# Optimization experiments

Measured on AMD Instinct MI355X. Metric: run time of the kernel, lower is better.

## Reference

```python
import jax, jax.numpy as jnp
import numpy as np

B = 1024
E = 512
NUM_HEADS = 8
EPS = 1e-5  # torch LayerNorm default


def _mha(x, w_qkv, b_qkv, w_o, b_o):
    """torch nn.MultiheadAttention (batch_first, self-attn, no dropout).
    x: [N, S, E]; w_qkv: [3E, E]; w_o: [E, E]."""
    N, S, Ex = x.shape
    H = NUM_HEADS
    D = Ex // H
    qkv = x @ w_qkv.T + b_qkv                      # [N, S, 3E]
    q, k, v = jnp.split(qkv, 3, axis=-1)
    q = q.reshape(N, S, H, D).transpose(0, 2, 1, 3)  # [N, H, S, D]
    k = k.reshape(N, S, H, D).transpose(0, 2, 1, 3)
    v = v.reshape(N, S, H, D).transpose(0, 2, 1, 3)
    scores = jnp.einsum('nhqd,nhkd->nhqk', q, k) * (D ** -0.5)
    attn = jax.nn.softmax(scores, axis=-1)
    out = jnp.einsum('nhqk,nhkd->nhqd', attn, v)
    out = out.transpose(0, 2, 1, 3).reshape(N, S, Ex)
    return out @ w_o.T + b_o


def _box_perm(g):
    """Permute 9x9 grid so each 3x3 box becomes a contiguous row of 9.
    This permutation is its own inverse. g: [B, 9, 9, E]."""
    Bx = g.shape[0]
    return (g.reshape(Bx, 3, 3, 3, 3, E)
             .transpose(0, 1, 3, 2, 4, 5)
             .reshape(Bx, 9, 9, E))


def setup_inputs() -> dict:
    key = jax.random.key(0)
    ks = jax.random.split(key, 16)
    s = 0.02
    inp = {'x': jax.random.normal(ks[0], (B, 81, E), jnp.float32)}
    for i, p in enumerate(['row', 'col', 'box']):
        inp[p + '_wqkv'] = jax.random.normal(ks[1 + 2 * i], (3 * E, E), jnp.float32) * s
        inp[p + '_bqkv'] = jnp.zeros((3 * E,), jnp.float32)
        inp[p + '_wo'] = jax.random.normal(ks[2 + 2 * i], (E, E), jnp.float32) * s
        inp[p + '_bo'] = jnp.zeros((E,), jnp.float32)
    inp['w1'] = jax.random.normal(ks[7], (2 * E, 3 * E), jnp.float32) * s
    inp['b1'] = jnp.zeros((2 * E,), jnp.float32)
    inp['w2'] = jax.random.normal(ks[8], (E, 2 * E), jnp.float32) * s
    inp['b2'] = jnp.zeros((E,), jnp.float32)
    inp['gamma'] = jnp.ones((E,), jnp.float32)
    inp['beta'] = jnp.zeros((E,), jnp.float32)
    return inp


def reference(x, row_wqkv, row_bqkv, row_wo, row_bo,
              col_wqkv, col_bqkv, col_wo, col_bo,
              box_wqkv, box_bqkv, box_wo, box_bo,
              w1, b1, w2, b2, gamma, beta):
    Bx = x.shape[0]
    # Row attention: rows are already contiguous groups of 9.
    row_out = _mha(x.reshape(Bx * 9, 9, E), row_wqkv, row_bqkv, row_wo, row_bo)
    row_out = row_out.reshape(Bx, 81, E)
    # Column attention: transpose grid so columns are contiguous.
    col_x = x.reshape(Bx, 9, 9, E).transpose(0, 2, 1, 3).reshape(Bx * 9, 9, E)
    col_out = _mha(col_x, col_wqkv, col_bqkv, col_wo, col_bo)
    col_out = col_out.reshape(Bx, 9, 9, E).transpose(0, 2, 1, 3).reshape(Bx, 81, E)
    # Box attention: permute grid so each 3x3 box is contiguous.
    box_x = _box_perm(x.reshape(Bx, 9, 9, E)).reshape(Bx * 9, 9, E)
    box_out = _mha(box_x, box_wqkv, box_bqkv, box_wo, box_bo)
    box_out = _box_perm(box_out.reshape(Bx, 9, 9, E)).reshape(Bx, 81, E)
    # Constraint mixer MLP.
    combined = jnp.concatenate([row_out, col_out, box_out], axis=-1)  # [B,81,3E]
    h = jax.nn.gelu(combined @ w1.T + b1, approximate=False)
    mixed = h @ w2.T + b2
    # Residual + LayerNorm.
    y = x + mixed
    mu = jnp.mean(y, axis=-1, keepdims=True)
    var = jnp.var(y, axis=-1, keepdims=True)
    return (y - mu) * jax.lax.rsqrt(var + EPS) * gamma + beta
```

## Files before the change

### kernel.cpp

```cpp
#include <hip/hip_runtime.h>
#include <hip/hip_bf16.h>
#include <math.h>

typedef __hip_bfloat16 bf16;
typedef __attribute__((ext_vector_type(8))) short s8v;
typedef __attribute__((ext_vector_type(4))) short s4v;
typedef __attribute__((ext_vector_type(4))) float f4v;

static __device__ __forceinline__ float bfs2f(short s) {
    return __uint_as_float(((unsigned)(unsigned short)s) << 16);
}
static __device__ __forceinline__ short f2bfs(float f) {
    __hip_bfloat16 h = __float2bfloat16(f);
    return *reinterpret_cast<short*>(&h);
}

__global__ __launch_bounds__(256)
void cvt_f32_bf16(const float* __restrict__ in, bf16* __restrict__ out, long n4)
{
    const long i = (long)blockIdx.x * 256 + threadIdx.x;
    if (i >= n4) return;
    const float4 v = reinterpret_cast<const float4*>(in)[i];
    s4v o;
    o[0] = f2bfs(v.x); o[1] = f2bfs(v.y); o[2] = f2bfs(v.z); o[3] = f2bfs(v.w);
    reinterpret_cast<s4v*>(out)[i] = o;
}

__global__ __launch_bounds__(256)
void cvt_t_f32_bf16(const float* __restrict__ in, bf16* __restrict__ out,
                    int R, int C)
{
    __shared__ float t[32][33];
    const int bx = blockIdx.x * 32;
    const int by = blockIdx.y * 32;
    const int tx = threadIdx.x & 31;
    const int ty = threadIdx.x >> 5;
#pragma unroll
    for (int r = ty; r < 32; r += 8)
        t[r][tx] = in[(long)(by + r) * C + bx + tx];
    __syncthreads();
#pragma unroll
    for (int r = ty; r < 32; r += 8)
        out[(long)(bx + r) * R + by + tx] = __float2bfloat16(t[tx][r]);
}

__global__ __launch_bounds__(256)
void fold_b1(const float* __restrict__ w1, const float* __restrict__ bo0,
             const float* __restrict__ bo1, const float* __restrict__ bo2,
             const float* __restrict__ b1, float* __restrict__ b1p)
{
    const int m = blockIdx.x * 256 + threadIdx.x;
    float s = b1[m];
    const float* w = w1 + (long)m * 1536;
    for (int k = 0; k < 512; ++k) s += w[k]        * bo0[k];
    for (int k = 0; k < 512; ++k) s += w[512 + k]  * bo1[k];
    for (int k = 0; k < 512; ++k) s += w[1024 + k] * bo2[k];
    b1p[m] = s;
}

template<int ACT>
__global__ __launch_bounds__(512, 2)
void gemm256(const bf16* __restrict__ A, const bf16* __restrict__ B,
             const float* __restrict__ bias, bf16* __restrict__ C,
             int K, int lda, int ldc, int coff)
{
    __shared__ __align__(16) bf16 sA[2][256 * 64];
    __shared__ __align__(16) bf16 sB[2][256 * 64];
    const int tid  = threadIdx.x;
    const int lane = tid & 63;
    const int wid  = tid >> 6;
    const int nwg  = gridDim.x * gridDim.y;
    const int orig = blockIdx.x + gridDim.x * blockIdx.y;
    const int q = nwg >> 3, r = nwg & 7, xcd = orig & 7;
    const int sb = (xcd < r ? xcd * (q + 1) : r * (q + 1) + (xcd - r) * q) + (orig >> 3);
    const int bCol = sb % gridDim.x;
    const int bRow = sb / gridDim.x;

    const int wr  = (wid >> 2) * 128;
    const int wc  = (wid & 3) * 64;
    const int fr  = lane & 15;
    const int hi4 = lane >> 4;
    const int rx  = fr & 7;

    f4v acc[8][4];
#pragma unroll
    for (int i = 0; i < 8; ++i)
#pragma unroll
        for (int j = 0; j < 4; ++j) acc[i][j] = (f4v)(0.0f);

    const int srow = tid >> 3;
    const int scol = ((tid & 7) ^ (srow & 7)) * 8;
    const bf16* Abase = A + (long)(bRow * 256 + srow) * lda + scol;
    const bf16* Bbase = B + (long)(bCol * 256 + srow) * K + scol;

#define GL16(src, dst)                                                          \
    __builtin_amdgcn_global_load_lds(                                           \
        (const __attribute__((address_space(1))) unsigned int*)(src),           \
        (__attribute__((address_space(3))) unsigned int*)(dst), 16, 0, 0)

#define STAGE_A(h, tt, bc) do {                                                 \
    const bf16* g_ = Abase + (long)(h) * 128 * lda + (long)(tt) * 64;           \
    char* d_ = (char*)sA[bc] + (h) * 16384 + tid * 16;                          \
    GL16(g_, d_); GL16(g_ + 64 * (long)lda, d_ + 8192); } while (0)

#define STAGE_B(h, tt, bc) do {                                                 \
    const bf16* g_ = Bbase + (long)(h) * 128 * K + (long)(tt) * 64;             \
    char* d_ = (char*)sB[bc] + (h) * 16384 + tid * 16;                          \
    GL16(g_, d_); GL16(g_ + 64 * (long)K, d_ + 8192); } while (0)

#define LDSW(base, row, kk)                                                     \
    (*(const s8v*)((base) + (row) * 128 + ((((kk) * 4 + hi4) ^ rx) << 4)))

    const int nk = K >> 6;

    STAGE_A(0, 0, 0); STAGE_A(1, 0, 0);
    STAGE_B(0, 0, 0); STAGE_B(1, 0, 0);
    STAGE_B(0, 1, 1); STAGE_B(1, 1, 1);
    asm volatile("s_waitcnt vmcnt(4)" ::: "memory");
    __builtin_amdgcn_s_barrier();
    __builtin_amdgcn_sched_barrier(0);

    for (int t = 0; t < nk; ++t) {
        const int c = t & 1;
        const char* sAc = (const char*)sA[c];
        const char* sBc = (const char*)sB[c];
        s8v bfr[4][2];

        {
            s8v af0[2][2], af1[2][2];
#pragma unroll
            for (int m2 = 0; m2 < 2; ++m2)
#pragma unroll
                for (int kk = 0; kk < 2; ++kk) {
                    af0[m2][kk] = LDSW(sAc, wr + m2 * 16 + fr, kk);
                    af1[m2][kk] = LDSW(sAc, wr + (2 + m2) * 16 + fr, kk);
                }
#pragma unroll
            for (int ni = 0; ni < 4; ++ni)
#pragma unroll
                for (int kk = 0; kk < 2; ++kk)
                    bfr[ni][kk] = LDSW(sBc, wc + ni * 16 + fr, kk);
            if (t + 1 < nk) { STAGE_A(0, t + 1, c ^ 1); STAGE_A(1, t + 1, c ^ 1); }
            __builtin_amdgcn_s_setprio(1);
#pragma unroll
            for (int kk = 0; kk < 2; ++kk)
#pragma unroll
                for (int m2 = 0; m2 < 2; ++m2)
#pragma unroll
                    for (int ni = 0; ni < 4; ++ni) {
                        acc[m2][ni] = __builtin_amdgcn_mfma_f32_16x16x32_bf16(
                            af0[m2][kk], bfr[ni][kk], acc[m2][ni], 0, 0, 0);
                        acc[2 + m2][ni] = __builtin_amdgcn_mfma_f32_16x16x32_bf16(
                            af1[m2][kk], bfr[ni][kk], acc[2 + m2][ni], 0, 0, 0);
                    }
            __builtin_amdgcn_s_setprio(0);
        }
        __builtin_amdgcn_s_barrier();

        {
            s8v af0[2][2], af1[2][2];
#pragma unroll
            for (int m2 = 0; m2 < 2; ++m2)
#pragma unroll
                for (int kk = 0; kk < 2; ++kk) {
                    af0[m2][kk] = LDSW(sAc, wr + (4 + m2) * 16 + fr, kk);
                    af1[m2][kk] = LDSW(sAc, wr + (6 + m2) * 16 + fr, kk);
                }
            if (t + 2 < nk) { STAGE_B(0, t + 2, c); STAGE_B(1, t + 2, c); }
            __builtin_amdgcn_s_setprio(1);
#pragma unroll
            for (int kk = 0; kk < 2; ++kk)
#pragma unroll
                for (int m2 = 0; m2 < 2; ++m2)
#pragma unroll
                    for (int ni = 0; ni < 4; ++ni) {
                        acc[4 + m2][ni] = __builtin_amdgcn_mfma_f32_16x16x32_bf16(
                            af0[m2][kk], bfr[ni][kk], acc[4 + m2][ni], 0, 0, 0);
                        acc[6 + m2][ni] = __builtin_amdgcn_mfma_f32_16x16x32_bf16(
                            af1[m2][kk], bfr[ni][kk], acc[6 + m2][ni], 0, 0, 0);
                    }
            __builtin_amdgcn_s_setprio(0);
        }
        if (t + 2 < nk) {
            asm volatile("s_waitcnt vmcnt(4)" ::: "memory");
        } else if (t + 1 < nk) {
            asm volatile("s_waitcnt vmcnt(0)" ::: "memory");
        }
        __builtin_amdgcn_s_barrier();
        __builtin_amdgcn_sched_barrier(0);
    }
#undef STAGE_A
#undef STAGE_B
#undef GL16
#undef LDSW

    const int frow = hi4 * 4;
    const long rowBase = (long)bRow * 256 + wr;
    const int  colBase = bCol * 256 + wc;
#pragma unroll
    for (int ni = 0; ni < 4; ++ni) {
        const int col = colBase + ni * 16 + fr;
        const float bi = bias ? bias[coff + col] : 0.0f;
#pragma unroll
        for (int mi = 0; mi < 8; ++mi) {
#pragma unroll
            for (int j = 0; j < 4; ++j) {
                float v = acc[mi][ni][j] + bi;
                if (ACT == 1) {
                    const float u = v * (0.7978845608f + 0.0356774081f * v * v);
                    const float tnh = 1.0f - 2.0f / (__expf(2.0f * u) + 1.0f);
                    v = 0.5f * v * (1.0f + tnh);
                }
                const long rr = rowBase + mi * 16 + frow + j;
                C[rr * (long)ldc + coff + col] = __float2bfloat16(v);
            }
        }
    }
}

__global__ __launch_bounds__(256)
void attn9(const bf16* __restrict__ qkv, bf16* __restrict__ outg,
           long chunk_base)
{
    __shared__ __align__(16) bf16 sQKV[9 * 1536];
    __shared__ float sP[8 * 81];
    __shared__ int sTok[9];
    const int tid = threadIdx.x;
    const int branch = blockIdx.y;
    const int bx = blockIdx.x;
    const int s = (bx & 7) * (2304 >> 3) + (bx >> 3);
    const int b = s / 9, g = s % 9;

    if (tid < 9) {
        const int p = tid;
        int cell;
        if (branch == 0)      cell = g * 9 + p;
        else if (branch == 1) cell = p * 9 + g;
        else                  cell = ((g / 3) * 3 + p / 3) * 9 + (g % 3) * 3 + (p % 3);
        sTok[p] = b * 81 + cell;
    }
    __syncthreads();

    const long brOff = (long)branch * 1536;
    for (int c = tid; c < 1728; c += 256) {
        const int p = c / 192;
        const int off = (c - p * 192) * 8;
        *(s8v*)(&sQKV[p * 1536 + off]) =
            *(const s8v*)(&qkv[(long)sTok[p] * 4608 + brOff + off]);
    }
    __syncthreads();

    for (int t = tid; t < 648; t += 256) {
        const int h = t / 81;
        const int r = t - h * 81;
        const int i = r / 9, j = r - (r / 9) * 9;
        const bf16* qp = &sQKV[i * 1536 + h * 64];
        const bf16* kp = &sQKV[j * 1536 + 512 + h * 64];
        float accd = 0.0f;
#pragma unroll
        for (int dc = 0; dc < 8; ++dc) {
            s8v qv = *(const s8v*)(qp + dc * 8);
            s8v kv = *(const s8v*)(kp + dc * 8);
#pragma unroll
            for (int e2 = 0; e2 < 8; ++e2)
                accd += bfs2f(qv[e2]) * bfs2f(kv[e2]);
        }
        sP[t] = accd * 0.125f;
    }
    __syncthreads();

    if (tid < 72) {
        float* row = &sP[tid * 9];
        float m = row[0];
#pragma unroll
        for (int j = 1; j < 9; ++j) m = fmaxf(m, row[j]);
        float sum = 0.f, e[9];
#pragma unroll
        for (int j = 0; j < 9; ++j) { e[j] = expf(row[j] - m); sum += e[j]; }
        const float inv = 1.0f / sum;
#pragma unroll
        for (int j = 0; j < 9; ++j) row[j] = e[j] * inv;
    }
    __syncthreads();

    for (int t = tid; t < 576; t += 256) {
        const int i = t >> 6;
        const int c8 = (t & 63) * 8;
        const int h = (t & 63) >> 3;
        const float* prow = &sP[h * 81 + i * 9];
        float accv[8];
#pragma unroll
        for (int q2 = 0; q2 < 8; ++q2) accv[q2] = 0.f;
#pragma unroll
        for (int j = 0; j < 9; ++j) {
            const float p = prow[j];
            s8v vv = *(const s8v*)(&sQKV[j * 1536 + 1024 + c8]);
#pragma unroll
            for (int q2 = 0; q2 < 8; ++q2)
                accv[q2] += p * bfs2f(vv[q2]);
        }
        s8v ov;
#pragma unroll
        for (int q2 = 0; q2 < 8; ++q2) ov[q2] = f2bfs(accv[q2]);
        *(s8v*)(&outg[(chunk_base + sTok[i]) * 1536 + branch * 512 + c8]) = ov;
    }
}

__global__ __launch_bounds__(256)
void ln_res(const float* __restrict__ x, const bf16* __restrict__ mixed,
            const float* __restrict__ gamma, const float* __restrict__ beta,
            float* __restrict__ out)
{
    const int tid = threadIdx.x;
    const int lane = tid & 63;
    const long row = (long)blockIdx.x * 4 + (tid >> 6);
    const long base = row * 512 + lane * 8;
    const float4 x0 = *(const float4*)(&x[base]);
    const float4 x1 = *(const float4*)(&x[base + 4]);
    const s8v mv = *(const s8v*)(&mixed[base]);
    float y[8];
    y[0] = x0.x + bfs2f(mv[0]); y[1] = x0.y + bfs2f(mv[1]);
    y[2] = x0.z + bfs2f(mv[2]); y[3] = x0.w + bfs2f(mv[3]);
    y[4] = x1.x + bfs2f(mv[4]); y[5] = x1.y + bfs2f(mv[5]);
    y[6] = x1.z + bfs2f(mv[6]); y[7] = x1.w + bfs2f(mv[7]);
    float sum = 0.f, sq = 0.f;
#pragma unroll
    for (int j = 0; j < 8; ++j) { sum += y[j]; sq += y[j] * y[j]; }
#pragma unroll
    for (int o = 32; o > 0; o >>= 1) {
        sum += __shfl_xor(sum, o, 64);
        sq  += __shfl_xor(sq, o, 64);
    }
    const float mean = sum * (1.f / 512.f);
    const float inv = rsqrtf(sq * (1.f / 512.f) - mean * mean + 1e-5f);
    const float4 g0 = *(const float4*)(&gamma[lane * 8]);
    const float4 g1 = *(const float4*)(&gamma[lane * 8 + 4]);
    const float4 b0 = *(const float4*)(&beta[lane * 8]);
    const float4 b1 = *(const float4*)(&beta[lane * 8 + 4]);
    float4 o0, o1;
    o0.x = (y[0] - mean) * inv * g0.x + b0.x;
    o0.y = (y[1] - mean) * inv * g0.y + b0.y;
    o0.z = (y[2] - mean) * inv * g0.z + b0.z;
    o0.w = (y[3] - mean) * inv * g0.w + b0.w;
    o1.x = (y[4] - mean) * inv * g1.x + b1.x;
    o1.y = (y[5] - mean) * inv * g1.y + b1.y;
    o1.z = (y[6] - mean) * inv * g1.z + b1.z;
    o1.w = (y[7] - mean) * inv * g1.w + b1.w;
    *(float4*)(&out[base]) = o0;
    *(float4*)(&out[base + 4]) = o1;
}

extern "C" void kernel_launch(void* const* d_in, const int* in_sizes, int n_in,
                              void* d_out, int out_size, void* d_ws, size_t ws_size,
                              hipStream_t stream)
{
    (void)in_sizes; (void)n_in; (void)out_size; (void)ws_size;
    const float* x     = (const float*)d_in[0];
    const float* w1f   = (const float*)d_in[13];
    const float* b1f   = (const float*)d_in[14];
    const float* b2f   = (const float*)d_in[16];
    const float* gamma = (const float*)d_in[17];
    const float* beta  = (const float*)d_in[18];

    char* ws = (char*)d_ws;
    bf16* attnall   = (bf16*)(ws);
    bf16* mixed     = (bf16*)(ws);
    char* R         = ws + 254803968LL;
    bf16* qkv3chunk = (bf16*)(R);
    bf16* xb        = (bf16*)(R + 191102976LL);
    bf16* h         = (bf16*)(R);
    char* wb        = ws + 530841600LL;
    long off = 0;
    bf16* wqkv3_b = (bf16*)(wb + off); off += 4718592;
    bf16* woT_b[3];
    for (int i = 0; i < 3; ++i) { woT_b[i] = (bf16*)(wb + off); off += 524288; }
    bf16* w1_b  = (bf16*)(wb + off); off += 3145728;
    bf16* w2_b  = (bf16*)(wb + off); off += 1048576;
    bf16* Wp    = (bf16*)(wb + off); off += 3145728;
    float* b1p  = (float*)(wb + off); off += 4096;
    float* bqkv3 = (float*)(wb + off); off += 18432;

    const dim3 blk(256, 1, 1);
    const dim3 blk512(512, 1, 1);

    cvt_f32_bf16<<<dim3(41472), blk, 0, stream>>>(x, xb, 10616832L);
    for (int i = 0; i < 3; ++i) {
        cvt_f32_bf16<<<dim3(768), blk, 0, stream>>>(
            (const float*)d_in[1 + i * 4], wqkv3_b + (long)i * 786432, 196608L);
        cvt_t_f32_bf16<<<dim3(16, 16), blk, 0, stream>>>(
            (const float*)d_in[3 + i * 4], woT_b[i], 512, 512);
        hipMemcpyAsync(bqkv3 + i * 1536, d_in[2 + i * 4], 1536 * sizeof(float),
                       hipMemcpyDeviceToDevice, stream);
    }
    cvt_f32_bf16<<<dim3(1536), blk, 0, stream>>>(w1f, w1_b, 393216L);
    cvt_f32_bf16<<<dim3(512), blk, 0, stream>>>((const float*)d_in[15], w2_b, 131072L);

    fold_b1<<<dim3(4), blk, 0, stream>>>(w1f, (const float*)d_in[4],
                                         (const float*)d_in[8], (const float*)d_in[12],
                                         b1f, b1p);

    for (int br = 0; br < 3; ++br)
        gemm256<0><<<dim3(2, 4), blk512, 0, stream>>>(
            w1_b + br * 512, woT_b[br], nullptr, Wp, 512, 1536, 1536, br * 512);

    const long ROWS_C = 20736;
    for (int c = 0; c < 4; ++c) {
        const bf16* xA = xb + c * ROWS_C * 512;
        gemm256<0><<<dim3(18, 81), blk512, 0, stream>>>(
            xA, wqkv3_b, bqkv3, qkv3chunk, 512, 512, 4608, 0);
        attn9<<<dim3(2304, 3), blk, 0, stream>>>(qkv3chunk, attnall, c * ROWS_C);
    }
    gemm256<1><<<dim3(4, 324), blk512, 0, stream>>>(attnall, Wp, b1p, h, 1536, 1536, 1024, 0);
    gemm256<0><<<dim3(2, 324), blk512, 0, stream>>>(h, w2_b, b2f, mixed, 1024, 1024, 512, 0);
    ln_res<<<dim3(20736), blk, 0, stream>>>(x, mixed, gamma, beta, (float*)d_out);
}
```

Measured before the change: 1.564 ms.

## Stage GEMM epilogue through LDS and split attn9 work per wave

```diff
diff --git a/kernel.cpp b/kernel.cpp
--- a/kernel.cpp
+++ b/kernel.cpp
@@ -194,6 +194,9 @@
 #undef GL16
 #undef LDSW
 
+    __syncthreads();
+    bf16* ep = (wid < 4) ? ((bf16*)sA + wid * 8192)
+                         : ((bf16*)sB + (wid - 4) * 8192);
     const int frow = hi4 * 4;
     const long rowBase = (long)bRow * 256 + wr;
     const int  colBase = bCol * 256 + wc;
@@ -211,66 +214,89 @@
                     const float tnh = 1.0f - 2.0f / (__expf(2.0f * u) + 1.0f);
                     v = 0.5f * v * (1.0f + tnh);
                 }
-                const long rr = rowBase + mi * 16 + frow + j;
-                C[rr * (long)ldc + coff + col] = __float2bfloat16(v);
+                ep[(mi * 16 + frow + j) * 64 + ni * 16 + fr] = __float2bfloat16(v);
             }
         }
     }
+    asm volatile("s_waitcnt lgkmcnt(0)" ::: "memory");
+    __builtin_amdgcn_sched_barrier(0);
+    const int lr8 = lane >> 3;
+    const int lc  = (lane & 7) * 8;
+#pragma unroll
+    for (int q2 = 0; q2 < 16; ++q2) {
+        const int lrow = q2 * 8 + lr8;
+        const s8v vv = *(const s8v*)(&ep[lrow * 64 + lc]);
+        *(s8v*)(&C[(rowBase + lrow) * (long)ldc + coff + colBase + lc]) = vv;
+    }
+}
+
+__device__ __forceinline__ int cell9(int branch, int g, int p)
+{
+    if (branch == 0) return g * 9 + p;
+    if (branch == 1) return p * 9 + g;
+    return ((g / 3) * 3 + p / 3) * 9 + (g % 3) * 3 + (p % 3);
 }
 
 __global__ __launch_bounds__(256)
 void attn9(const bf16* __restrict__ qkv, bf16* __restrict__ outg,
            long chunk_base)
 {
-    __shared__ __align__(16) bf16 sQKV[9 * 1536];
-    __shared__ float sP[8 * 81];
-    __shared__ int sTok[9];
-    const int tid = threadIdx.x;
+    __shared__ __align__(16) bf16 sW[4 * 9 * 392];
+    __shared__ float sP[4][2][84];
+    const int tid  = threadIdx.x;
+    const int lane = tid & 63;
+    const int w    = tid >> 6;
     const int branch = blockIdx.y;
     const int bx = blockIdx.x;
     const int s = (bx & 7) * (2304 >> 3) + (bx >> 3);
     const int b = s / 9, g = s % 9;
-
-    if (tid < 9) {
-        const int p = tid;
-        int cell;
-        if (branch == 0)      cell = g * 9 + p;
-        else if (branch == 1) cell = p * 9 + g;
-        else                  cell = ((g / 3) * 3 + p / 3) * 9 + (g % 3) * 3 + (p % 3);
-        sTok[p] = b * 81 + cell;
-    }
-    __syncthreads();
-
     const long brOff = (long)branch * 1536;
-    for (int c = tid; c < 1728; c += 256) {
-        const int p = c / 192;
-        const int off = (c - p * 192) * 8;
-        *(s8v*)(&sQKV[p * 1536 + off]) =
-            *(const s8v*)(&qkv[(long)sTok[p] * 4608 + brOff + off]);
-    }
-    __syncthreads();
-
-    for (int t = tid; t < 648; t += 256) {
-        const int h = t / 81;
-        const int r = t - h * 81;
-        const int i = r / 9, j = r - (r / 9) * 9;
-        const bf16* qp = &sQKV[i * 1536 + h * 64];
-        const bf16* kp = &sQKV[j * 1536 + 512 + h * 64];
-        float accd = 0.0f;
-#pragma unroll
-        for (int dc = 0; dc < 8; ++dc) {
-            s8v qv = *(const s8v*)(qp + dc * 8);
-            s8v kv = *(const s8v*)(kp + dc * 8);
-#pragma unroll
-            for (int e2 = 0; e2 < 8; ++e2)
-                accd += bfs2f(qv[e2]) * bfs2f(kv[e2]);
-        }
-        sP[t] = accd * 0.125f;
-    }
-    __syncthreads();
-
-    if (tid < 72) {
-        float* row = &sP[tid * 9];
+    bf16* myW = sW + w * (9 * 392);
+
+#pragma unroll
+    for (int rr = 0; rr < 7; ++rr) {
+        const int c = rr * 64 + lane;
+        if (c < 432) {
+            const int p   = c / 48;
+            const int rem = c - p * 48;
+            const int seg = rem >> 3;
+            const int ch  = rem & 7;
+            const int col = (seg >> 1) * 512 + ((w << 1) + (seg & 1)) * 64 + ch * 8;
+            const long tok = b * 81 + cell9(branch, g, p);
+            *(s8v*)(&myW[p * 392 + seg * 64 + ch * 8]) =
+                *(const s8v*)(&qkv[tok * 4608 + brOff + col]);
+        }
+    }
+    asm volatile("s_waitcnt lgkmcnt(0) vmcnt(0)" ::: "memory");
+    __builtin_amdgcn_sched_barrier(0);
+
+#pragma unroll
+    for (int rr = 0; rr < 3; ++rr) {
+        const int idx = rr * 64 + lane;
+        if (idx < 162) {
+            const int h2 = idx / 81;
+            const int pr = idx - h2 * 81;
+            const int i = pr / 9, j = pr - (pr / 9) * 9;
+            const bf16* qp = &myW[i * 392 + h2 * 64];
+            const bf16* kp = &myW[j * 392 + 128 + h2 * 64];
+            float accd = 0.0f;
+#pragma unroll
+            for (int dc = 0; dc < 8; ++dc) {
+                s8v qv = *(const s8v*)(qp + dc * 8);
+                s8v kv = *(const s8v*)(kp + dc * 8);
+#pragma unroll
+                for (int e2 = 0; e2 < 8; ++e2)
+                    accd += bfs2f(qv[e2]) * bfs2f(kv[e2]);
+            }
+            sP[w][h2][pr] = accd * 0.125f;
+        }
+    }
+    asm volatile("s_waitcnt lgkmcnt(0)" ::: "memory");
+    __builtin_amdgcn_sched_barrier(0);
+
+    if (lane < 18) {
+        const int h2 = lane / 9, i = lane - (lane / 9) * 9;
+        float* row = &sP[w][h2][i * 9];
         float m = row[0];
 #pragma unroll
         for (int j = 1; j < 9; ++j) m = fmaxf(m, row[j]);
@@ -281,28 +307,36 @@
 #pragma unroll
         for (int j = 0; j < 9; ++j) row[j] = e[j] * inv;
     }
-    __syncthreads();
-
-    for (int t = tid; t < 576; t += 256) {
-        const int i = t >> 6;
-        const int c8 = (t & 63) * 8;
-        const int h = (t & 63) >> 3;
-        const float* prow = &sP[h * 81 + i * 9];
-        float accv[8];
-#pragma unroll
-        for (int q2 = 0; q2 < 8; ++q2) accv[q2] = 0.f;
-#pragma unroll
-        for (int j = 0; j < 9; ++j) {
-            const float p = prow[j];
-            s8v vv = *(const s8v*)(&sQKV[j * 1536 + 1024 + c8]);
-#pragma unroll
-            for (int q2 = 0; q2 < 8; ++q2)
-                accv[q2] += p * bfs2f(vv[q2]);
-        }
-        s8v ov;
-#pragma unroll
-        for (int q2 = 0; q2 < 8; ++q2) ov[q2] = f2bfs(accv[q2]);
-        *(s8v*)(&outg[(chunk_base + sTok[i]) * 1536 + branch * 512 + c8]) = ov;
+    asm volatile("s_waitcnt lgkmcnt(0)" ::: "memory");
+    __builtin_amdgcn_sched_barrier(0);
+
+#pragma unroll
+    for (int rr = 0; rr < 3; ++rr) {
+        const int idx = rr * 64 + lane;
+        if (idx < 144) {
+            const int h2  = idx / 72;
+            const int rem = idx - h2 * 72;
+            const int i  = rem >> 3;
+            const int c8 = (rem & 7) * 8;
+            const float* prow = &sP[w][h2][i * 9];
+            float accv[8];
+#pragma unroll
+            for (int q2 = 0; q2 < 8; ++q2) accv[q2] = 0.f;
+#pragma unroll
+            for (int j = 0; j < 9; ++j) {
+                const float p = prow[j];
+                const s8v vv = *(const s8v*)(&myW[j * 392 + 256 + h2 * 64 + c8]);
+#pragma unroll
+                for (int q2 = 0; q2 < 8; ++q2)
+                    accv[q2] += p * bfs2f(vv[q2]);
+            }
+            s8v ov;
+#pragma unroll
+            for (int q2 = 0; q2 < 8; ++q2) ov[q2] = f2bfs(accv[q2]);
+            const long tok = b * 81 + cell9(branch, g, i);
+            const int ocol = ((w << 1) + h2) * 64 + c8;
+            *(s8v*)(&outg[(chunk_base + tok) * 1536 + branch * 512 + ocol]) = ov;
+        }
     }
 }
 
```

New measurement: 1.425 ms, median of 2. 8.9% less time.
